# Kernel tuning notes

Measured on AMD Instinct MI355X. Metric: run time of the kernel, lower is better.

Reference implementation:

```python
import jax, jax.numpy as jnp
import numpy as np

NBINS = 256

def _equalize(image):
    # image: [B, C, H, W] float32 holding integer pixel values in [0, 255]
    B, C, H, W = image.shape
    flat = image.reshape(B * C, H * W)
    idx = flat.astype(jnp.int32)                      # pixel values as bin indices
    rows = jnp.arange(B * C, dtype=jnp.int32)[:, None]
    seg_ids = (rows * NBINS + idx).reshape(-1)
    # per-(batch,channel) 256-bin histogram via one segment_sum (scatter-add)
    hist = jax.ops.segment_sum(jnp.ones((B * C * H * W,), jnp.int32), seg_ids,
                               num_segments=B * C * NBINS).reshape(B * C, NBINS)
    # torchvision: step = nonzero_hist[:-1].sum() // 255
    #            = (total_count - last_nonzero_value) // 255
    bins = jnp.arange(NBINS, dtype=jnp.int32)
    last_idx = jnp.max(jnp.where(hist != 0, bins[None, :], -1), axis=1)  # [BC]
    last_val = jnp.take_along_axis(hist, jnp.maximum(last_idx, 0)[:, None], axis=1)[:, 0]
    total = hist.sum(axis=1)
    step = (total - last_val) // (NBINS - 1)          # [BC] int32
    safe_step = jnp.maximum(step, 1)                  # avoid div-by-zero; masked below
    # lut = (cumsum(hist) + step//2) // step, shifted right by 1 with 0, clamped
    cum = jnp.cumsum(hist, axis=1)
    lut = (cum + (step // 2)[:, None]) // safe_step[:, None]
    lut = jnp.concatenate([jnp.zeros((B * C, 1), lut.dtype), lut[:, :-1]], axis=1)
    lut = jnp.clip(lut, 0, 255)
    remapped = jnp.take_along_axis(lut, idx, axis=1).astype(image.dtype)
    # if step == 0, channel is returned unchanged
    out = jnp.where((step == 0)[:, None], flat, remapped)
    return out.reshape(B, C, H, W)

def setup_inputs() -> dict:
    key = jax.random.key(0)
    u = jax.random.uniform(key, (32, 3, 1024, 1024), dtype=jnp.float32)
    image = jnp.clip(jnp.floor(u * 256.0), 0.0, 255.0)  # integer-valued pixels
    return {"image": image}

def reference(image) -> jnp.ndarray:
    return _equalize(image)
```

## Files before the change

kernel.cpp:

```cpp
#include <hip/hip_runtime.h>

#define NBINS 256
#define CHANNELS 96
#define PIX_PER_CH (1024 * 1024)
#define CHUNKS 64
#define PIX_PER_BLOCK (PIX_PER_CH / CHUNKS)
#define THREADS 256
#define V4_PER_THREAD (PIX_PER_BLOCK / 4 / THREADS)

__global__ __launch_bounds__(THREADS) void hist_kernel(
    const float* __restrict__ in, int* __restrict__ hist) {
    __shared__ int sh[4][NBINS];
    const int t = threadIdx.x;
    const int wave = t >> 6;

    for (int i = t; i < 4 * NBINS; i += THREADS) ((int*)sh)[i] = 0;
    __syncthreads();

    const int c = blockIdx.x / CHUNKS;
    const int chunk = blockIdx.x % CHUNKS;
    const float4* in4 =
        (const float4*)(in + (size_t)c * PIX_PER_CH + (size_t)chunk * PIX_PER_BLOCK);

#pragma unroll
    for (int i = 0; i < V4_PER_THREAD; ++i) {
        float4 v = in4[i * THREADS + t];
        atomicAdd(&sh[wave][(int)v.x], 1);
        atomicAdd(&sh[wave][(int)v.y], 1);
        atomicAdd(&sh[wave][(int)v.z], 1);
        atomicAdd(&sh[wave][(int)v.w], 1);
    }
    __syncthreads();

    int sum = sh[0][t] + sh[1][t] + sh[2][t] + sh[3][t];
    if (sum) atomicAdd(&hist[c * NBINS + t], sum);
}

__global__ __launch_bounds__(THREADS) void lut_kernel(
    const int* __restrict__ hist, float* __restrict__ lut) {
    __shared__ int sh[NBINS];
    __shared__ int scan[NBINS];
    __shared__ int red[NBINS];
    const int t = threadIdx.x;
    const int c = blockIdx.x;

    const int h = hist[c * NBINS + t];
    sh[t] = h;
    int val = h;
    scan[t] = val;
    red[t] = (h != 0) ? t : -1;
    __syncthreads();

#pragma unroll
    for (int off = 1; off < NBINS; off <<= 1) {
        int add = (t >= off) ? scan[t - off] : 0;
        __syncthreads();
        val += add;
        scan[t] = val;
        __syncthreads();
    }

#pragma unroll
    for (int off = NBINS / 2; off > 0; off >>= 1) {
        if (t < off) red[t] = max(red[t], red[t + off]);
        __syncthreads();
    }

    const int last_idx = red[0];
    const int total = scan[NBINS - 1];
    const int last_val = sh[last_idx];
    const int step = (total - last_val) / (NBINS - 1);

    float out;
    if (step == 0) {
        out = (float)t;
    } else {
        int v = (t == 0) ? 0 : (scan[t - 1] + (step >> 1)) / step;
        out = (float)min(v, 255);
    }
    lut[c * NBINS + t] = out;
}

__global__ __launch_bounds__(THREADS) void remap_kernel(
    const float* __restrict__ in, const float* __restrict__ lut,
    float* __restrict__ out) {
    __shared__ float slut[NBINS];
    const int t = threadIdx.x;
    const int c = blockIdx.x / CHUNKS;
    const int chunk = blockIdx.x % CHUNKS;

    slut[t] = lut[c * NBINS + t];
    __syncthreads();

    const size_t base = (size_t)c * PIX_PER_CH + (size_t)chunk * PIX_PER_BLOCK;
    const float4* in4 = (const float4*)(in + base);
    float4* out4 = (float4*)(out + base);

#pragma unroll
    for (int i = 0; i < V4_PER_THREAD; ++i) {
        float4 v = in4[i * THREADS + t];
        float4 r;
        r.x = slut[(int)v.x];
        r.y = slut[(int)v.y];
        r.z = slut[(int)v.z];
        r.w = slut[(int)v.w];
        out4[i * THREADS + t] = r;
    }
}

extern "C" void kernel_launch(void* const* d_in, const int* in_sizes, int n_in,
                              void* d_out, int out_size, void* d_ws, size_t ws_size,
                              hipStream_t stream) {
    const float* image = (const float*)d_in[0];
    float* out = (float*)d_out;

    int* hist = (int*)d_ws;
    float* lut = (float*)((char*)d_ws + CHANNELS * NBINS * sizeof(int));

    hipMemsetAsync(hist, 0, CHANNELS * NBINS * sizeof(int), stream);

    hist_kernel<<<CHANNELS * CHUNKS, THREADS, 0, stream>>>(image, hist);
    lut_kernel<<<CHANNELS, THREADS, 0, stream>>>(hist, lut);
    remap_kernel<<<CHANNELS * CHUNKS, THREADS, 0, stream>>>(image, lut, out);
}
```

Before: 724.5 us.

## Pack pixel bytes during histogram pass and remap from packed buffer

The histogram kernel now also writes each pixel's bin index as a packed byte into a workspace buffer, and the remap kernel reads these bytes instead of re-reading the float image. This cuts the second full-size float read down to a quarter-size byte read, at the cost of an extra write. The LUT kernel is rewritten as a single wavefront using shuffle scans and a ballot, and nontemporal load and store hints are added. It requires a workspace of about one byte per pixel.

```diff
diff --git a/kernel.cpp b/kernel.cpp
--- a/kernel.cpp
+++ b/kernel.cpp
@@ -6,10 +6,14 @@
 #define CHUNKS 64
 #define PIX_PER_BLOCK (PIX_PER_CH / CHUNKS)
 #define THREADS 256
-#define V4_PER_THREAD (PIX_PER_BLOCK / 4 / THREADS)
+#define W_PER_BLOCK (PIX_PER_BLOCK / 4)
+#define W_PER_THREAD (W_PER_BLOCK / THREADS)
 
-__global__ __launch_bounds__(THREADS) void hist_kernel(
-    const float* __restrict__ in, int* __restrict__ hist) {
+typedef float float4v __attribute__((ext_vector_type(4)));
+
+__global__ __launch_bounds__(THREADS) void hist_pack_kernel(
+    const float* __restrict__ in, unsigned int* __restrict__ packed,
+    int* __restrict__ hist) {
     __shared__ int sh[4][NBINS];
     const int t = threadIdx.x;
     const int wave = t >> 6;
@@ -17,18 +21,23 @@
     for (int i = t; i < 4 * NBINS; i += THREADS) ((int*)sh)[i] = 0;
     __syncthreads();
 
-    const int c = blockIdx.x / CHUNKS;
-    const int chunk = blockIdx.x % CHUNKS;
-    const float4* in4 =
-        (const float4*)(in + (size_t)c * PIX_PER_CH + (size_t)chunk * PIX_PER_BLOCK);
+    const int c = blockIdx.x >> 6;
+    const int chunk = blockIdx.x & 63;
+    const size_t base4 =
+        (size_t)c * (PIX_PER_CH / 4) + (size_t)chunk * W_PER_BLOCK;
+    const float4v* in4 = (const float4v*)in + base4;
+    unsigned int* w4 = packed + base4;
 
 #pragma unroll
-    for (int i = 0; i < V4_PER_THREAD; ++i) {
-        float4 v = in4[i * THREADS + t];
-        atomicAdd(&sh[wave][(int)v.x], 1);
-        atomicAdd(&sh[wave][(int)v.y], 1);
-        atomicAdd(&sh[wave][(int)v.z], 1);
-        atomicAdd(&sh[wave][(int)v.w], 1);
+    for (int i = 0; i < W_PER_THREAD; ++i) {
+        float4v v = __builtin_nontemporal_load(in4 + i * THREADS + t);
+        unsigned b0 = (unsigned)v.x, b1 = (unsigned)v.y;
+        unsigned b2 = (unsigned)v.z, b3 = (unsigned)v.w;
+        atomicAdd(&sh[wave][b0], 1);
+        atomicAdd(&sh[wave][b1], 1);
+        atomicAdd(&sh[wave][b2], 1);
+        atomicAdd(&sh[wave][b3], 1);
+        w4[i * THREADS + t] = b0 | (b1 << 8) | (b2 << 16) | (b3 << 24);
     }
     __syncthreads();
 
@@ -36,75 +45,73 @@
     if (sum) atomicAdd(&hist[c * NBINS + t], sum);
 }
 
-__global__ __launch_bounds__(THREADS) void lut_kernel(
+__global__ __launch_bounds__(64) void lut_kernel(
     const int* __restrict__ hist, float* __restrict__ lut) {
-    __shared__ int sh[NBINS];
-    __shared__ int scan[NBINS];
-    __shared__ int red[NBINS];
     const int t = threadIdx.x;
     const int c = blockIdx.x;
 
-    const int h = hist[c * NBINS + t];
-    sh[t] = h;
-    int val = h;
-    scan[t] = val;
-    red[t] = (h != 0) ? t : -1;
-    __syncthreads();
+    int4 h = ((const int4*)(hist + c * NBINS))[t];
+    const int s0 = h.x, s1 = s0 + h.y, s2 = s1 + h.z, s3 = s2 + h.w;
 
+    int incl = s3;
 #pragma unroll
-    for (int off = 1; off < NBINS; off <<= 1) {
-        int add = (t >= off) ? scan[t - off] : 0;
-        __syncthreads();
-        val += add;
-        scan[t] = val;
-        __syncthreads();
+    for (int off = 1; off < 64; off <<= 1) {
+        int n = __shfl_up(incl, off);
+        if (t >= off) incl += n;
     }
+    const int excl = incl - s3;
+    const int c0 = excl + s0, c1 = excl + s1, c2 = excl + s2, c3 = excl + s3;
 
-#pragma unroll
-    for (int off = NBINS / 2; off > 0; off >>= 1) {
-        if (t < off) red[t] = max(red[t], red[t + off]);
-        __syncthreads();
-    }
+    const int total = __shfl(incl, 63);
 
-    const int last_idx = red[0];
-    const int total = scan[NBINS - 1];
-    const int last_val = sh[last_idx];
+    unsigned long long nz = __ballot(h.x | h.y | h.z | h.w);
+    const int last_lane = 63 - __clzll(nz);
+    const int lv = h.w ? h.w : (h.z ? h.z : (h.y ? h.y : h.x));
+    const int last_val = __shfl(lv, last_lane);
+
     const int step = (total - last_val) / (NBINS - 1);
 
-    float out;
+    float o0, o1, o2, o3;
     if (step == 0) {
-        out = (float)t;
+        o0 = (float)(4 * t);
+        o1 = (float)(4 * t + 1);
+        o2 = (float)(4 * t + 2);
+        o3 = (float)(4 * t + 3);
     } else {
-        int v = (t == 0) ? 0 : (scan[t - 1] + (step >> 1)) / step;
-        out = (float)min(v, 255);
+        const int half = step >> 1;
+        int p = __shfl_up(c3, 1);
+        int prev = t ? p : 0;
+        o0 = (t == 0) ? 0.0f : (float)min((prev + half) / step, 255);
+        o1 = (float)min((c0 + half) / step, 255);
+        o2 = (float)min((c1 + half) / step, 255);
+        o3 = (float)min((c2 + half) / step, 255);
     }
-    lut[c * NBINS + t] = out;
+    float4v r = {o0, o1, o2, o3};
+    ((float4v*)(lut + c * NBINS))[t] = r;
 }
 
 __global__ __launch_bounds__(THREADS) void remap_kernel(
-    const float* __restrict__ in, const float* __restrict__ lut,
+    const unsigned int* __restrict__ packed, const float* __restrict__ lut,
     float* __restrict__ out) {
     __shared__ float slut[NBINS];
     const int t = threadIdx.x;
-    const int c = blockIdx.x / CHUNKS;
-    const int chunk = blockIdx.x % CHUNKS;
+    const int c = blockIdx.x >> 6;
+    const int chunk = blockIdx.x & 63;
 
     slut[t] = lut[c * NBINS + t];
     __syncthreads();
 
-    const size_t base = (size_t)c * PIX_PER_CH + (size_t)chunk * PIX_PER_BLOCK;
-    const float4* in4 = (const float4*)(in + base);
-    float4* out4 = (float4*)(out + base);
+    const size_t base4 =
+        (size_t)c * (PIX_PER_CH / 4) + (size_t)chunk * W_PER_BLOCK;
+    const unsigned int* w4 = packed + base4;
+    float4v* out4 = (float4v*)out + base4;
 
 #pragma unroll
-    for (int i = 0; i < V4_PER_THREAD; ++i) {
-        float4 v = in4[i * THREADS + t];
-        float4 r;
-        r.x = slut[(int)v.x];
-        r.y = slut[(int)v.y];
-        r.z = slut[(int)v.z];
-        r.w = slut[(int)v.w];
-        out4[i * THREADS + t] = r;
+    for (int i = 0; i < W_PER_THREAD; ++i) {
+        unsigned w = w4[i * THREADS + t];
+        float4v r = {slut[w & 255], slut[(w >> 8) & 255], slut[(w >> 16) & 255],
+                     slut[w >> 24]};
+        __builtin_nontemporal_store(r, out4 + i * THREADS + t);
     }
 }
 
@@ -114,12 +121,14 @@
     const float* image = (const float*)d_in[0];
     float* out = (float*)d_out;
 
-    int* hist = (int*)d_ws;
-    float* lut = (float*)((char*)d_ws + CHANNELS * NBINS * sizeof(int));
+    unsigned int* packed = (unsigned int*)d_ws;
+    char* base = (char*)d_ws + (size_t)CHANNELS * PIX_PER_CH;
+    int* hist = (int*)base;
+    float* lut = (float*)(base + CHANNELS * NBINS * sizeof(int));
 
     hipMemsetAsync(hist, 0, CHANNELS * NBINS * sizeof(int), stream);
 
-    hist_kernel<<<CHANNELS * CHUNKS, THREADS, 0, stream>>>(image, hist);
-    lut_kernel<<<CHANNELS, THREADS, 0, stream>>>(hist, lut);
-    remap_kernel<<<CHANNELS * CHUNKS, THREADS, 0, stream>>>(image, lut, out);
+    hist_pack_kernel<<<CHANNELS * CHUNKS, THREADS, 0, stream>>>(image, packed, hist);
+    lut_kernel<<<CHANNELS, 64, 0, stream>>>(hist, lut);
+    remap_kernel<<<CHANNELS * CHUNKS, THREADS, 0, stream>>>(packed, lut, out);
 }
```

New measurement: 645.4 us. 10.9% less time.
